# Performance work log

Measured on AMD Instinct MI355X. Metric: run time of the kernel, lower is better.

Reference implementation:

```python
import jax, jax.numpy as jnp
import numpy as np

BATCH = 32768
DIM = 256
NUM_LATENTS = 4096
ENTROPY_WEIGHT = 0.1
VQ_BETA = 0.25
EPS = 1e-9


def _l2_normalize(v, axis=-1, eps=1e-12):
    # matches torch F.normalize(dim=-1)
    n = jnp.linalg.norm(v, axis=axis, keepdims=True)
    return v / jnp.maximum(n, eps)


def setup_inputs() -> dict:
    key = jax.random.key(0)
    kx, kc = jax.random.split(key)
    x = jax.random.normal(kx, (BATCH, DIM), dtype=jnp.float32)
    # codebook initialized uniform(-bound, bound) then row-normalized, as in __init__
    bound = (3.0 / DIM) ** 0.5
    cb = jax.random.uniform(kc, (NUM_LATENTS, DIM), dtype=jnp.float32,
                            minval=-bound, maxval=bound)
    codebook = _l2_normalize(cb)
    return {"x": x, "codebook": codebook}


def reference(x, codebook):
    # cosine-distance nearest-code lookup
    x_norm = _l2_normalize(x)                       # [B, D]
    cb_norm = _l2_normalize(codebook)               # [K, D]
    distance = -jnp.einsum('bd,kd->bk', x_norm, cb_norm)  # [B, K]
    # dropout p=0.0 -> identity
    indices = jnp.argmin(distance, axis=-1)         # [B] int
    z = codebook[indices]                           # [B, D] gather

    # straight-through estimator
    z_q = x + jax.lax.stop_gradient(z - x)

    commit_loss = jnp.mean((x - jax.lax.stop_gradient(z)) ** 2)
    q_loss = jnp.mean((z - jax.lax.stop_gradient(x)) ** 2)

    # entropy of codebook usage
    counts = jnp.bincount(indices, length=NUM_LATENTS).astype(jnp.float32)
    probs = counts / counts.sum()
    entropy = -jnp.sum(probs * jnp.log(jnp.clip(probs, EPS)))
    entropy_loss = -entropy

    vq_loss = q_loss + VQ_BETA * commit_loss + ENTROPY_WEIGHT * entropy_loss
    return (z_q, vq_loss, q_loss, commit_loss, entropy_loss, entropy, indices)
```

## Files before the change

### kernel.cpp

```cpp
#include <hip/hip_runtime.h>
#include <math.h>

#define BATCH 32768
#define DIM   256
#define NLAT  4096

typedef _Float16 f16x8 __attribute__((ext_vector_type(8)));
typedef float    f32x16 __attribute__((ext_vector_type(16)));

#define WS_CBH    0u
#define WS_CBINV  2097152u
#define WS_KEYS   2113536u
#define WS_HIST   4210688u

__device__ inline float kdec(uint key) {
  return __uint_as_float(key & 0xFFFFF000u);
}

__device__ inline void gload_lds16(const void* g, void* l) {
  __builtin_amdgcn_global_load_lds(
      (const __attribute__((address_space(1))) void*)g,
      (__attribute__((address_space(3))) void*)l, 16, 0, 0);
}

__global__ __launch_bounds__(256) void prep1_kernel(
    const float* __restrict__ cb, float* __restrict__ cbinv,
    int* __restrict__ hist) {
  int bid = blockIdx.x;
  if (bid < 1024) {
    int w = threadIdx.x >> 6, l = threadIdx.x & 63;
    int row = bid * 4 + w;
    const float4* cr = (const float4*)(cb + (size_t)row * DIM);
    float4 v = cr[l];
    float s = v.x * v.x + v.y * v.y + v.z * v.z + v.w * v.w;
    #pragma unroll
    for (int m = 32; m; m >>= 1) s += __shfl_xor(s, m, 64);
    if (l == 0) cbinv[row] = 1.0f / fmaxf(sqrtf(s), 1e-12f);
  } else {
    for (int k = threadIdx.x; k < NLAT; k += 256) hist[k] = 0;
  }
}

__global__ __launch_bounds__(256) void prep2_kernel(
    const float* __restrict__ x, const float* __restrict__ cb,
    const float* __restrict__ cbinv, uint4* __restrict__ cbhf4,
    uint4* __restrict__ xhf4) {
  int bid = blockIdx.x, tid = threadIdx.x;
  if (bid < 512) {
    int gid = bid * 256 + tid;
    int frag = gid >> 6, lane = gid & 63;
    int rf = frag & 1, ts = frag >> 1, sl = ts & 15, t = ts >> 4;
    int row = t * 64 + rf * 32 + (lane & 31);
    int e4 = sl * 4 + (lane >> 5) * 2;
    const float4* cr = (const float4*)(cb + (size_t)row * DIM);
    float inv = cbinv[row];
    float4 a = cr[e4], b = cr[e4 + 1];
    union { _Float16 h[8]; uint4 u; } pk;
    pk.h[0] = (_Float16)(a.x * inv); pk.h[1] = (_Float16)(a.y * inv);
    pk.h[2] = (_Float16)(a.z * inv); pk.h[3] = (_Float16)(a.w * inv);
    pk.h[4] = (_Float16)(b.x * inv); pk.h[5] = (_Float16)(b.y * inv);
    pk.h[6] = (_Float16)(b.z * inv); pk.h[7] = (_Float16)(b.w * inv);
    cbhf4[gid] = pk.u;
  } else {
    int o = (bid - 512) * 256 + tid;
    int rowgrp = o >> 10, rem = o & 1023;
    int sl = rem >> 6, rem2 = rem & 63;
    int lhh = rem2 >> 5, l31r = rem2 & 31;
    int row = rowgrp * 32 + l31r;
    int c = sl * 2 + lhh;
    const float4* xs = (const float4*)x;
    float4 a = xs[(size_t)row * 64 + c * 2];
    float4 b = xs[(size_t)row * 64 + c * 2 + 1];
    union { _Float16 h[8]; uint4 u; } pk;
    pk.h[0] = (_Float16)a.x; pk.h[1] = (_Float16)a.y;
    pk.h[2] = (_Float16)a.z; pk.h[3] = (_Float16)a.w;
    pk.h[4] = (_Float16)b.x; pk.h[5] = (_Float16)b.y;
    pk.h[6] = (_Float16)b.z; pk.h[7] = (_Float16)b.w;
    xhf4[o] = pk.u;
  }
}

__global__ __launch_bounds__(256, 2) void vq_gemm_kernel(
    const char* __restrict__ xhf, const char* __restrict__ cbhf,
    uint* __restrict__ keys) {
  __shared__ __align__(16) char smem[65536];

  const int tid = threadIdx.x;
  const int w = tid >> 6, l = tid & 63;
  const int l31 = l & 31, lh = l >> 5;
  const int bb = blockIdx.x >> 2, q = blockIdx.x & 3;
  const int wrow0 = bb * 128 + w * 32;
  const int cbase = q * 1024;
  const uint lh4u = (uint)(lh << 2);

  const char* xb = xhf + ((size_t)(bb * 4 + w) * 1024 + l) * 16;
  f16x8 xf[16];
  #pragma unroll
  for (int s2 = 0; s2 < 16; ++s2) xf[s2] = *(const f16x8*)(xb + s2 * 1024);

  const char* qbase = cbhf + (size_t)q * 524288;
  auto STAGE = [&](int bufoff, int t) {
    const char* src = qbase + t * 32768 + (size_t)tid * 16;
    char* dst = smem + bufoff + w * 1024;
    #pragma unroll
    for (int s = 0; s < 8; ++s)
      gload_lds16(src + s * 4096, dst + s * 4096);
  };

  STAGE(0, 0);
  asm volatile("s_waitcnt vmcnt(0)" ::: "memory");
  __syncthreads();

  uint k1 = 0, k2 = 0, k3 = 0;
  int curoff = 0;

  #pragma unroll 1
  for (int t = 0; t < 16; ++t) {
    if (t < 15) STAGE(curoff ^ 32768, t + 1);

    f32x16 acc[2];
    #pragma unroll
    for (int r = 0; r < 16; ++r) { acc[0][r] = 32.0f; acc[1][r] = 32.0f; }

    const char* bp = smem + curoff + (size_t)l * 16;
    #pragma unroll
    for (int sl = 0; sl < 16; ++sl) {
      f16x8 a0 = *(const f16x8*)(bp + (sl * 2) * 1024);
      f16x8 a1 = *(const f16x8*)(bp + (sl * 2 + 1) * 1024);
      acc[0] = __builtin_amdgcn_mfma_f32_32x32x16_f16(
          a0, xf[sl], acc[0], 0, 0, 0);
      acc[1] = __builtin_amdgcn_mfma_f32_32x32x16_f16(
          a1, xf[sl], acc[1], 0, 0, 0);
    }

    const uint scode = (uint)(cbase + t * 64);
    #pragma unroll
    for (int rf = 0; rf < 2; ++rf) {
      #pragma unroll
      for (int r = 0; r < 16; ++r) {
        const uint cr = (uint)(rf * 32 + (r & 3) + 8 * (r >> 2));
        uint key = (__float_as_uint(acc[rf][r]) & 0xFFFFF000u)
                 | scode | cr | lh4u;
        uint m1 = max(k1, key), n1 = min(k1, key); k1 = m1;
        uint m2 = max(k2, n1),  n2 = min(k2, n1);  k2 = m2;
        k3 = max(k3, n2);
      }
    }

    asm volatile("s_waitcnt vmcnt(0)" ::: "memory");
    __syncthreads();
    curoff ^= 32768;
  }

  uint o1 = __shfl_xor(k1, 32, 64);
  uint o2 = __shfl_xor(k2, 32, 64);
  uint o3 = __shfl_xor(k3, 32, 64);
  uint k4 = 0;
  #pragma unroll
  for (int e = 0; e < 3; ++e) {
    uint o = (e == 0) ? o1 : (e == 1) ? o2 : o3;
    uint m = max(k1, o), n = min(k1, o); k1 = m;
    m = max(k2, n); n = min(k2, n); k2 = m;
    m = max(k3, n); n = min(k3, n); k3 = m;
    k4 = max(k4, n);
  }
  if (lh == 0) {
    uint4 kv; kv.x = k1; kv.y = k2; kv.z = k3; kv.w = k4;
    *(uint4*)(keys + (size_t)(wrow0 + l31) * 16 + q * 4) = kv;
  }
}

__global__ __launch_bounds__(256) void rescore_kernel(
    const float* __restrict__ x, const float* __restrict__ cb,
    const float* __restrict__ cbinv, const uint* __restrict__ keys,
    float* __restrict__ zq, float* __restrict__ out_idx,
    int* __restrict__ hist, double* __restrict__ psse) {
  __shared__ float part[4];
  int tid = threadIdx.x, w = tid >> 6, l = tid & 63;
  int row = blockIdx.x * 4 + w;
  const float4* xr = (const float4*)(x + (size_t)row * DIM);
  float4 xv = xr[l];
  float s0 = xv.x * xv.x + xv.y * xv.y + xv.z * xv.z + xv.w * xv.w;
  #pragma unroll
  for (int m = 32; m; m >>= 1) s0 += __shfl_xor(s0, m, 64);
  float xnorm = sqrtf(s0);
  float xinv = 1.0f / fmaxf(xnorm, 1e-12f);

  uint key = keys[row * 16 + (l & 15)];
  uint kmax = key;
  #pragma unroll
  for (int m = 1; m < 16; m <<= 1) {
    uint o = __shfl_xor(kmax, m, 64);
    kmax = (o > kmax) ? o : kmax;
  }
  float dmax = kdec(kmax);
  float thr = dmax - 2.0f * (3e-3f * xnorm);
  bool inwin = (kdec(key) >= thr) && (l < 16);
  unsigned long long mask = __ballot(inwin);
  int besti;
  if (__popcll(mask) == 1) {
    besti = (int)(kmax & 0xFFFu);
  } else {
    float bestv = -3e38f; besti = 0x7fffffff;
    unsigned long long mm = mask;
    while (mm) {
      int b = __ffsll(mm) - 1; mm &= mm - 1;
      int ci = (int)(__shfl(key, b, 64) & 0xFFFu);
      float cbi = cbinv[ci];
      const float4* cr = (const float4*)(cb + (size_t)ci * DIM);
      float4 cv = cr[l];
      float d = (xv.x * xinv) * (cv.x * cbi) + (xv.y * xinv) * (cv.y * cbi)
              + (xv.z * xinv) * (cv.z * cbi) + (xv.w * xinv) * (cv.w * cbi);
      #pragma unroll
      for (int m = 32; m; m >>= 1) d += __shfl_xor(d, m, 64);
      bool better = (d > bestv) || (d == bestv && ci < besti);
      bestv = better ? d : bestv;
      besti = better ? ci : besti;
    }
  }

  float4 zv = ((const float4*)(cb + (size_t)besti * DIM))[l];
  float4 o;
  o.x = xv.x + (zv.x - xv.x); o.y = xv.y + (zv.y - xv.y);
  o.z = xv.z + (zv.z - xv.z); o.w = xv.w + (zv.w - xv.w);
  ((float4*)(zq + (size_t)row * DIM))[l] = o;
  float dx = xv.x - zv.x, dy = xv.y - zv.y, dz = xv.z - zv.z, dw = xv.w - zv.w;
  float s = dx * dx + dy * dy + dz * dz + dw * dw;
  #pragma unroll
  for (int m = 32; m; m >>= 1) s += __shfl_xor(s, m, 64);
  if (l == 0) part[w] = s;
  __syncthreads();
  if (tid == 0)
    psse[blockIdx.x] = (double)((part[0] + part[1]) + (part[2] + part[3]));
  if (l == 0) {
    atomicAdd(&hist[besti], 1);
    out_idx[row] = (float)besti;
  }
}

__global__ __launch_bounds__(256) void finalize_kernel(
    const int* __restrict__ hist, const double* __restrict__ psse,
    float* __restrict__ outs) {
  int tid = threadIdx.x;
  double e = 0.0, s = 0.0;
  for (int k = tid; k < NLAT; k += 256) {
    int c = hist[k];
    if (c > 0) {
      float p = (float)c * (1.0f / 32768.0f);
      e += (double)(p * logf(p));
    }
  }
  for (int k = tid; k < BATCH / 4; k += 256) s += psse[k];
  #pragma unroll
  for (int off = 32; off; off >>= 1) {
    e += __shfl_xor(e, off, 64);
    s += __shfl_xor(s, off, 64);
  }
  __shared__ double pe[4], ps[4];
  int w = tid >> 6, l = tid & 63;
  if (l == 0) { pe[w] = e; ps[w] = s; }
  __syncthreads();
  if (tid == 0) {
    double H = -((pe[0] + pe[1]) + (pe[2] + pe[3]));
    double sse = (ps[0] + ps[1]) + (ps[2] + ps[3]);
    double qv = sse * (1.0 / ((double)BATCH * (double)DIM));
    float qf = (float)qv;
    float Hf = (float)H;
    float ent_loss = -Hf;
    float vq = qf + 0.25f * qf + 0.1f * ent_loss;
    outs[0] = vq;
    outs[1] = qf;
    outs[2] = qf;
    outs[3] = ent_loss;
    outs[4] = Hf;
  }
}

extern "C" void kernel_launch(void* const* d_in, const int* in_sizes, int n_in,
                              void* d_out, int out_size, void* d_ws, size_t ws_size,
                              hipStream_t stream) {
  const float* x  = (const float*)d_in[0];
  const float* cb = (const float*)d_in[1];

  float* out     = (float*)d_out;
  float* zq      = out;
  float* scalars = out + (size_t)BATCH * DIM;
  float* oidx    = scalars + 5;

  char* wsb = (char*)d_ws;
  ushort* cbhf  = (ushort*)(wsb + WS_CBH);
  float*  cbinv = (float*)(wsb + WS_CBINV);
  uint*   keys  = (uint*)(wsb + WS_KEYS);
  int*    hist  = (int*)(wsb + WS_HIST);
  double* psse  = (double*)(wsb + WS_CBH);

  ushort* xhf = (ushort*)d_out;

  prep1_kernel<<<1025, 256, 0, stream>>>(cb, cbinv, hist);
  prep2_kernel<<<4608, 256, 0, stream>>>(x, cb, cbinv,
                                         (uint4*)cbhf, (uint4*)xhf);
  vq_gemm_kernel<<<1024, 256, 0, stream>>>((const char*)xhf,
                                           (const char*)cbhf, keys);
  rescore_kernel<<<BATCH / 4, 256, 0, stream>>>(x, cb, cbinv, keys,
                                                zq, oidx, hist, psse);
  finalize_kernel<<<1, 256, 0, stream>>>(hist, psse, scalars);
}
```

Measured before the change: 201.6 us.

## Halve GEMM LDS stage size for higher occupancy and coalesce x fp16 packing via LDS

The GEMM kernel now stages half a codebook tile (16 KB) per pipeline step instead of 32 KB. Each 64-code tile is split across two K-halves with accumulators carried between them, and launch bounds rise from 2 to 4 blocks per CU. The x fp16 conversion in prep2 now reads contiguous rows, transposes them through LDS into the MFMA fragment layout, and writes coalesced output. The smaller stages double the number of barriers and async-wait points, and persistent accumulators plus 4-block occupancy may cause register pressure or spills.

```diff
diff --git a/kernel.cpp b/kernel.cpp
--- a/kernel.cpp
+++ b/kernel.cpp
@@ -46,8 +46,29 @@
     const float* __restrict__ cbinv, uint4* __restrict__ cbhf4,
     uint4* __restrict__ xhf4) {
   int bid = blockIdx.x, tid = threadIdx.x;
-  if (bid < 512) {
-    int gid = bid * 256 + tid;
+  if (bid < 1024) {
+    __shared__ __align__(16) uint4 lds[1024];
+    const float4* xs = (const float4*)x + (size_t)bid * 2048;
+    #pragma unroll
+    for (int k = 0; k < 4; ++k) {
+      int g = tid * 4 + k;
+      float4 a = xs[g * 2];
+      float4 b = xs[g * 2 + 1];
+      union { _Float16 h[8]; uint4 u; } pk;
+      pk.h[0] = (_Float16)a.x; pk.h[1] = (_Float16)a.y;
+      pk.h[2] = (_Float16)a.z; pk.h[3] = (_Float16)a.w;
+      pk.h[4] = (_Float16)b.x; pk.h[5] = (_Float16)b.y;
+      pk.h[6] = (_Float16)b.z; pk.h[7] = (_Float16)b.w;
+      int row31 = g >> 5, c = g & 31;
+      lds[(c >> 1) * 64 + (c & 1) * 32 + row31] = pk.u;
+    }
+    __syncthreads();
+    uint4* outp = xhf4 + (size_t)bid * 1024;
+    #pragma unroll
+    for (int k = 0; k < 4; ++k)
+      outp[tid * 4 + k] = lds[tid * 4 + k];
+  } else {
+    int gid = (bid - 1024) * 256 + tid;
     int frag = gid >> 6, lane = gid & 63;
     int rf = frag & 1, ts = frag >> 1, sl = ts & 15, t = ts >> 4;
     int row = t * 64 + rf * 32 + (lane & 31);
@@ -61,29 +82,13 @@
     pk.h[4] = (_Float16)(b.x * inv); pk.h[5] = (_Float16)(b.y * inv);
     pk.h[6] = (_Float16)(b.z * inv); pk.h[7] = (_Float16)(b.w * inv);
     cbhf4[gid] = pk.u;
-  } else {
-    int o = (bid - 512) * 256 + tid;
-    int rowgrp = o >> 10, rem = o & 1023;
-    int sl = rem >> 6, rem2 = rem & 63;
-    int lhh = rem2 >> 5, l31r = rem2 & 31;
-    int row = rowgrp * 32 + l31r;
-    int c = sl * 2 + lhh;
-    const float4* xs = (const float4*)x;
-    float4 a = xs[(size_t)row * 64 + c * 2];
-    float4 b = xs[(size_t)row * 64 + c * 2 + 1];
-    union { _Float16 h[8]; uint4 u; } pk;
-    pk.h[0] = (_Float16)a.x; pk.h[1] = (_Float16)a.y;
-    pk.h[2] = (_Float16)a.z; pk.h[3] = (_Float16)a.w;
-    pk.h[4] = (_Float16)b.x; pk.h[5] = (_Float16)b.y;
-    pk.h[6] = (_Float16)b.z; pk.h[7] = (_Float16)b.w;
-    xhf4[o] = pk.u;
-  }
-}
-
-__global__ __launch_bounds__(256, 2) void vq_gemm_kernel(
+  }
+}
+
+__global__ __launch_bounds__(256, 4) void vq_gemm_kernel(
     const char* __restrict__ xhf, const char* __restrict__ cbhf,
     uint* __restrict__ keys) {
-  __shared__ __align__(16) char smem[65536];
+  __shared__ __align__(16) char smem[32768];
 
   const int tid = threadIdx.x;
   const int w = tid >> 6, l = tid & 63;
@@ -93,17 +98,17 @@
   const int cbase = q * 1024;
   const uint lh4u = (uint)(lh << 2);
 
-  const char* xb = xhf + ((size_t)(bb * 4 + w) * 1024 + l) * 16;
+  const char* xb = xhf + (size_t)(bb * 4 + w) * 16384 + (size_t)l * 16;
   f16x8 xf[16];
   #pragma unroll
   for (int s2 = 0; s2 < 16; ++s2) xf[s2] = *(const f16x8*)(xb + s2 * 1024);
 
   const char* qbase = cbhf + (size_t)q * 524288;
-  auto STAGE = [&](int bufoff, int t) {
-    const char* src = qbase + t * 32768 + (size_t)tid * 16;
+  auto STAGE = [&](int bufoff, int h) {
+    const char* src = qbase + h * 16384 + (size_t)tid * 16;
     char* dst = smem + bufoff + w * 1024;
     #pragma unroll
-    for (int s = 0; s < 8; ++s)
+    for (int s = 0; s < 4; ++s)
       gload_lds16(src + s * 4096, dst + s * 4096);
   };
 
@@ -113,43 +118,48 @@
 
   uint k1 = 0, k2 = 0, k3 = 0;
   int curoff = 0;
+  f32x16 acc[2];
 
   #pragma unroll 1
-  for (int t = 0; t < 16; ++t) {
-    if (t < 15) STAGE(curoff ^ 32768, t + 1);
-
-    f32x16 acc[2];
-    #pragma unroll
-    for (int r = 0; r < 16; ++r) { acc[0][r] = 32.0f; acc[1][r] = 32.0f; }
+  for (int h = 0; h < 32; ++h) {
+    if (h < 31) STAGE(curoff ^ 16384, h + 1);
+
+    const int p = h & 1;
+    if (p == 0) {
+      #pragma unroll
+      for (int r = 0; r < 16; ++r) { acc[0][r] = 32.0f; acc[1][r] = 32.0f; }
+    }
 
     const char* bp = smem + curoff + (size_t)l * 16;
     #pragma unroll
-    for (int sl = 0; sl < 16; ++sl) {
-      f16x8 a0 = *(const f16x8*)(bp + (sl * 2) * 1024);
-      f16x8 a1 = *(const f16x8*)(bp + (sl * 2 + 1) * 1024);
+    for (int s8 = 0; s8 < 8; ++s8) {
+      f16x8 a0 = *(const f16x8*)(bp + (s8 * 2) * 1024);
+      f16x8 a1 = *(const f16x8*)(bp + (s8 * 2 + 1) * 1024);
       acc[0] = __builtin_amdgcn_mfma_f32_32x32x16_f16(
-          a0, xf[sl], acc[0], 0, 0, 0);
+          a0, xf[p * 8 + s8], acc[0], 0, 0, 0);
       acc[1] = __builtin_amdgcn_mfma_f32_32x32x16_f16(
-          a1, xf[sl], acc[1], 0, 0, 0);
-    }
-
-    const uint scode = (uint)(cbase + t * 64);
-    #pragma unroll
-    for (int rf = 0; rf < 2; ++rf) {
+          a1, xf[p * 8 + s8], acc[1], 0, 0, 0);
+    }
+
+    if (p == 1) {
+      const uint scode = (uint)(cbase + (h >> 1) * 64);
       #pragma unroll
-      for (int r = 0; r < 16; ++r) {
-        const uint cr = (uint)(rf * 32 + (r & 3) + 8 * (r >> 2));
-        uint key = (__float_as_uint(acc[rf][r]) & 0xFFFFF000u)
-                 | scode | cr | lh4u;
-        uint m1 = max(k1, key), n1 = min(k1, key); k1 = m1;
-        uint m2 = max(k2, n1),  n2 = min(k2, n1);  k2 = m2;
-        k3 = max(k3, n2);
+      for (int rf = 0; rf < 2; ++rf) {
+        #pragma unroll
+        for (int r = 0; r < 16; ++r) {
+          const uint cr = (uint)(rf * 32 + (r & 3) + 8 * (r >> 2));
+          uint key = (__float_as_uint(acc[rf][r]) & 0xFFFFF000u)
+                   | scode | cr | lh4u;
+          uint m1 = max(k1, key), n1 = min(k1, key); k1 = m1;
+          uint m2 = max(k2, n1),  n2 = min(k2, n1);  k2 = m2;
+          k3 = max(k3, n2);
+        }
       }
     }
 
     asm volatile("s_waitcnt vmcnt(0)" ::: "memory");
     __syncthreads();
-    curoff ^= 32768;
+    curoff ^= 16384;
   }
 
   uint o1 = __shfl_xor(k1, 32, 64);
@@ -297,7 +307,7 @@
   ushort* xhf = (ushort*)d_out;
 
   prep1_kernel<<<1025, 256, 0, stream>>>(cb, cbinv, hist);
-  prep2_kernel<<<4608, 256, 0, stream>>>(x, cb, cbinv,
+  prep2_kernel<<<1536, 256, 0, stream>>>(x, cb, cbinv,
                                          (uint4*)cbhf, (uint4*)xhf);
   vq_gemm_kernel<<<1024, 256, 0, stream>>>((const char*)xhf,
                                            (const char*)cbhf, keys);
```

After: 294.6 us. 1.46x slower.
